# Performance work log

Measured on AMD Instinct MI355X. Metric: run time of the kernel, lower is better.

Reference implementation:

```python
import math
import jax, jax.numpy as jnp
import numpy as np

B, A, U, S, E, HYP, H = 16384, 32, 64, 2048, 32, 64, 4
ATTEND_REG_COEF = 1e-3


def setup_inputs() -> dict:
    key = jax.random.key(0)
    ks = jax.random.split(key, 12)
    sc = 0.05
    return {
        "agent_qs": jax.random.normal(ks[0], (B, A), jnp.float32),
        "states": jax.random.normal(ks[1], (B, S), jnp.float32),
        # per-head selector hypernet: Linear(S,HYP)+ReLU+Linear(HYP,E,no bias)
        "sel_w1": jax.random.normal(ks[2], (H, S, HYP), jnp.float32) * sc,
        "sel_b1": jax.random.normal(ks[3], (H, HYP), jnp.float32) * sc,
        "sel_w2": jax.random.normal(ks[4], (H, HYP, E), jnp.float32) * sc,
        # per-head key extractor: Linear(U,E,no bias)
        "key_w": jax.random.normal(ks[5], (H, U, E), jnp.float32) * sc,
        # V net: Linear(S,E)+ReLU+Linear(E,1)
        "v_w1": jax.random.normal(ks[6], (S, E), jnp.float32) * sc,
        "v_b1": jax.random.normal(ks[7], (E,), jnp.float32) * sc,
        "v_w2": jax.random.normal(ks[8], (E, 1), jnp.float32) * sc,
        "v_b2": jax.random.normal(ks[9], (1,), jnp.float32) * sc,
    }


def reference(agent_qs, states, sel_w1, sel_b1, sel_w2, key_w, v_w1, v_b1, v_w2, v_b2):
    # nonlinear=False, weighted_head=False, state_bias=True (defaults used here)
    unit_states = states[:, : A * U].reshape(-1, A, U)  # [B, A, U]

    # per-head selectors: [B, H, E]
    h1 = jax.nn.relu(jnp.einsum("bs,hsk->bhk", states, sel_w1) + sel_b1[None])
    selectors = jnp.einsum("bhk,hke->bhe", h1, sel_w2)

    # per-head, per-agent keys: [B, H, A, E]
    keys = jnp.einsum("bau,hue->bhae", unit_states, key_w)

    # attention logits [B, H, A] (matches selector @ stacked-keys in torch)
    logits = jnp.einsum("bhe,bhae->bha", selectors, keys)
    weights = jax.nn.softmax(logits / math.sqrt(E), axis=-1)  # [B, H, A]

    head_attend = jnp.sum(weights, axis=1)  # [B, A]

    v = jax.nn.relu(states @ v_w1 + v_b1) @ v_w2 + v_b2  # [B, 1]

    # coef * sum over heads of mean(logits_h ** 2)
    attend_mag_regs = ATTEND_REG_COEF * jnp.sum(jnp.mean(logits ** 2, axis=(0, 2)))

    # per-head entropy: -(p * log(p + 1e-8)).sum(agents).mean(batch) -> [H]
    head_entropies = -jnp.mean(
        jnp.sum(weights * jnp.log(weights + 1e-8), axis=-1), axis=0
    )

    return head_attend, v, attend_mag_regs, head_entropies
```

## Files before the change

### kernel.cpp

```cpp
#include <hip/hip_runtime.h>
#include <hip/hip_bf16.h>

#define B_N 16384
#define A_N 32
#define U_N 64
#define S_N 2048
#define E_N 32
#define HYP_N 64
#define H_N 4
#define NREAL 288
#define NPADG 320

#define WS_WT    0
#define WS_MB    1310720
#define WS_PMAG  (WS_MB + 32768)
#define WS_PENT  (WS_PMAG + 65536)

#define OUT_V   (B_N * A_N)
#define OUT_MAG (OUT_V + B_N)
#define OUT_ENT (OUT_MAG + 1)

typedef __attribute__((ext_vector_type(8))) short bf16x8_t;
typedef __attribute__((ext_vector_type(4))) float floatx4_t;

#define AS1(p) ((const __attribute__((address_space(1))) void*)(p))
#define AS3(p) ((__attribute__((address_space(3))) void*)(p))

__device__ __forceinline__ unsigned short f2b(float f) {
    union { float f; unsigned u; } v; v.f = f;
    unsigned r = v.u + 0x7FFFu + ((v.u >> 16) & 1u);
    return (unsigned short)(r >> 16);
}
__device__ __forceinline__ float b2f(unsigned x) {
    union { unsigned u; float f; } v; v.u = x << 16; return v.f;
}

__global__ __launch_bounds__(256) void pack_w_kernel(
        const float* __restrict__ sel_w1, const float* __restrict__ v_w1,
        const float* __restrict__ sel_w2, const float* __restrict__ key_w,
        unsigned short* __restrict__ Wt, unsigned short* __restrict__ Mb) {
    int idx = blockIdx.x * 256 + threadIdx.x;
    if (idx < NPADG * S_N) {
        int n = idx >> 11;
        int k = idx & 2047;
        float val = 0.0f;
        if (n < 256) {
            int h = n >> 6, kk = n & 63;
            val = sel_w1[((size_t)h * S_N + k) * HYP_N + kk];
        } else if (n < NREAL) {
            val = v_w1[(size_t)k * E_N + (n - 256)];
        }
        Wt[idx] = f2b(val);
    } else if (idx < NPADG * S_N + H_N * U_N * HYP_N) {
        int j = idx - NPADG * S_N;
        int h = j >> 12, u = (j >> 6) & 63, k = j & 63;
        const float* kw = key_w + ((size_t)h * U_N + u) * E_N;
        const float* w2 = sel_w2 + ((size_t)h * HYP_N + k) * E_N;
        float s = 0.0f;
#pragma unroll
        for (int e = 0; e < E_N; ++e) s = fmaf(kw[e], w2[e], s);
        Mb[j] = f2b(s);
    }
}

#define FM_BM 32
#define FM_BK 64
#define H1_STRIDE 312
#define TS_STRIDE 260

__global__ __launch_bounds__(256) void fused_kernel(
        const float* __restrict__ states, const unsigned short* __restrict__ Wt,
        const float* __restrict__ sel_b1, const float* __restrict__ v_b1,
        const unsigned short* __restrict__ Mb,
        const float* __restrict__ v_w2, const float* __restrict__ v_b2,
        float* __restrict__ out, float* __restrict__ pmag, float* __restrict__ pent) {
    __shared__ __align__(16) char pool[4096 + 40960 + H1_STRIDE * FM_BM * 2];
    unsigned short* Asm = (unsigned short*)pool;
    unsigned short* Bsm = (unsigned short*)(pool + 4096);
    float*          tsb = (float*)(pool + 4096);
    unsigned short* h1b = (unsigned short*)(pool + 4096 + 40960);

    const int t = threadIdx.x;
    const int lane = t & 63;
    const int w = t >> 6;
    const int m0 = blockIdx.x * FM_BM;
    const int nw = w * 80;

    const int ar = t >> 3, acl = t & 7;
    const float* ap = states + (size_t)(m0 + ar) * S_N + acl * 8;

    floatx4_t acc[2][5] = {};

    float4 a0 = *(const float4*)(ap);
    float4 a1 = *(const float4*)(ap + 4);
    {
        int ph = acl ^ (ar & 7);
        uint4 o;
        o.x = (unsigned)f2b(a0.x) | ((unsigned)f2b(a0.y) << 16);
        o.y = (unsigned)f2b(a0.z) | ((unsigned)f2b(a0.w) << 16);
        o.z = (unsigned)f2b(a1.x) | ((unsigned)f2b(a1.y) << 16);
        o.w = (unsigned)f2b(a1.z) | ((unsigned)f2b(a1.w) << 16);
        *(uint4*)(Asm + (size_t)(ar * 8 + ph) * 8) = o;
    }
#pragma unroll
    for (int i = 0; i < 10; ++i) {
        int p = i * 256 + t, n = p >> 3, sl = p & 7;
        int cl = sl ^ (n & 7);
        __builtin_amdgcn_global_load_lds(AS1(Wt + (size_t)n * S_N + cl * 8),
                                         AS3(Bsm + p * 8), 16, 0, 0);
    }
    __syncthreads();

    for (int it = 0; it < 32; ++it) {
        if (it < 31) {
            const float* g = ap + (it + 1) * FM_BK;
            a0 = *(const float4*)(g);
            a1 = *(const float4*)(g + 4);
        }
#pragma unroll
        for (int s = 0; s < 2; ++s) {
            const int c = s * 4 + (lane >> 4);
            bf16x8_t afr[2];
#pragma unroll
            for (int mt = 0; mt < 2; ++mt) {
                int r = mt * 16 + (lane & 15);
                int ph = c ^ (r & 7);
                afr[mt] = *(const bf16x8_t*)(Asm + r * 64 + ph * 8);
            }
#pragma unroll
            for (int nt = 0; nt < 5; ++nt) {
                int n = nw + nt * 16 + (lane & 15);
                int ph = c ^ (n & 7);
                bf16x8_t bfr = *(const bf16x8_t*)(Bsm + n * 64 + ph * 8);
                acc[0][nt] = __builtin_amdgcn_mfma_f32_16x16x32_bf16(
                    afr[0], bfr, acc[0][nt], 0, 0, 0);
                acc[1][nt] = __builtin_amdgcn_mfma_f32_16x16x32_bf16(
                    afr[1], bfr, acc[1][nt], 0, 0, 0);
            }
        }
        __syncthreads();
        if (it < 31) {
            int k0 = (it + 1) * FM_BK;
            {
                int ph = acl ^ (ar & 7);
                uint4 o;
                o.x = (unsigned)f2b(a0.x) | ((unsigned)f2b(a0.y) << 16);
                o.y = (unsigned)f2b(a0.z) | ((unsigned)f2b(a0.w) << 16);
                o.z = (unsigned)f2b(a1.x) | ((unsigned)f2b(a1.y) << 16);
                o.w = (unsigned)f2b(a1.z) | ((unsigned)f2b(a1.w) << 16);
                *(uint4*)(Asm + (size_t)(ar * 8 + ph) * 8) = o;
            }
#pragma unroll
            for (int i = 0; i < 10; ++i) {
                int p = i * 256 + t, n = p >> 3, sl = p & 7;
                int cl = sl ^ (n & 7);
                __builtin_amdgcn_global_load_lds(
                    AS1(Wt + (size_t)n * S_N + k0 + cl * 8),
                    AS3(Bsm + p * 8), 16, 0, 0);
            }
            __syncthreads();
        }
    }

#pragma unroll
    for (int nt = 0; nt < 5; ++nt) {
        int n = nw + nt * 16 + (lane & 15);
        if (n >= NREAL) continue;
        float bias = (n < 256) ? sel_b1[n] : v_b1[n - 256];
        int slot = (n < 256) ? ((n >> 6) * 72 + (n & 63))
                             : (((n - 256) >> 3) * 72 + 64 + ((n - 256) & 7));
#pragma unroll
        for (int mt = 0; mt < 2; ++mt) {
#pragma unroll
            for (int rg = 0; rg < 4; ++rg) {
                int r = mt * 16 + (lane >> 4) * 4 + rg;
                float v = acc[mt][nt][rg] + bias;
                h1b[r * H1_STRIDE + slot] = f2b(v > 0.0f ? v : 0.0f);
            }
        }
    }
    __syncthreads();

    {
        const int h = w;
        floatx4_t tacc[2][4] = {};
#pragma unroll
        for (int s = 0; s < 2; ++s) {
            int k0 = s * 32 + (lane >> 4) * 8;
            bf16x8_t bfr[4];
#pragma unroll
            for (int ut = 0; ut < 4; ++ut) {
                int u = ut * 16 + (lane & 15);
                bfr[ut] = *(const bf16x8_t*)(Mb + ((size_t)(h * U_N + u) * 64) + k0);
            }
#pragma unroll
            for (int mt = 0; mt < 2; ++mt) {
                int r = mt * 16 + (lane & 15);
                bf16x8_t afr = *(const bf16x8_t*)(h1b + r * H1_STRIDE + h * 72 + k0);
#pragma unroll
                for (int ut = 0; ut < 4; ++ut)
                    tacc[mt][ut] = __builtin_amdgcn_mfma_f32_16x16x32_bf16(
                        afr, bfr[ut], tacc[mt][ut], 0, 0, 0);
            }
        }
#pragma unroll
        for (int mt = 0; mt < 2; ++mt)
#pragma unroll
            for (int ut = 0; ut < 4; ++ut)
#pragma unroll
                for (int rg = 0; rg < 4; ++rg) {
                    int r = mt * 16 + (lane >> 4) * 4 + rg;
                    int u = ut * 16 + (lane & 15);
                    tsb[r * TS_STRIDE + h * U_N + u] = tacc[mt][ut][rg];
                }
    }
    __syncthreads();

    const int a = lane & 31, uh = lane >> 5;
    float4 cur[8], nxt[8];
    {
        const float* up = states + (size_t)(m0 + w * 8) * S_N + a * 64 + uh * 32;
#pragma unroll
        for (int i = 0; i < 8; ++i) cur[i] = ((const float4*)up)[i];
    }
    for (int rr = 0; rr < 8; ++rr) {
        int r = w * 8 + rr;
        int b = m0 + r;
        if (rr < 7) {
            const float* up = states + (size_t)(b + 1) * S_N + a * 64 + uh * 32;
#pragma unroll
            for (int i = 0; i < 8; ++i) nxt[i] = ((const float4*)up)[i];
        }
        float pl[4];
#pragma unroll
        for (int h = 0; h < 4; ++h) {
            const float* tp = &tsb[r * TS_STRIDE + h * U_N + uh * 32];
            float s = 0.0f;
#pragma unroll
            for (int i = 0; i < 8; ++i) {
                float4 t4 = *(const float4*)(tp + i * 4);
                s = fmaf(cur[i].x, t4.x, s);
                s = fmaf(cur[i].y, t4.y, s);
                s = fmaf(cur[i].z, t4.z, s);
                s = fmaf(cur[i].w, t4.w, s);
            }
            pl[h] = s + __shfl_xor(s, 32, 64);
        }
        float mg = pl[0]*pl[0] + pl[1]*pl[1] + pl[2]*pl[2] + pl[3]*pl[3];
#pragma unroll
        for (int o = 16; o > 0; o >>= 1) mg += __shfl_xor(mg, o, 32);
        float hatt = 0.0f;
        float entv[4];
#pragma unroll
        for (int h = 0; h < 4; ++h) {
            float x = pl[h] * 0.17677669529663687f;
            float m = x;
#pragma unroll
            for (int o = 16; o > 0; o >>= 1) m = fmaxf(m, __shfl_xor(m, o, 32));
            float p = expf(x - m);
            float den = p;
#pragma unroll
            for (int o = 16; o > 0; o >>= 1) den += __shfl_xor(den, o, 32);
            float wv = p / den;
            hatt += wv;
            float e = wv * logf(wv + 1e-8f);
#pragma unroll
            for (int o = 16; o > 0; o >>= 1) e += __shfl_xor(e, o, 32);
            entv[h] = e;
        }
        if (uh == 0) {
            out[(size_t)b * A_N + a] = hatt;
            float pv = b2f((unsigned)h1b[r * H1_STRIDE + (a >> 3) * 72 + 64 + (a & 7)])
                       * v_w2[a];
#pragma unroll
            for (int o = 16; o > 0; o >>= 1) pv += __shfl_xor(pv, o, 32);
            if (a == 0) {
                out[OUT_V + b] = pv + v_b2[0];
                pmag[b] = mg;
#pragma unroll
                for (int h = 0; h < 4; ++h) pent[(size_t)h * B_N + b] = entv[h];
            }
        }
#pragma unroll
        for (int i = 0; i < 8; ++i) cur[i] = nxt[i];
    }
}

__global__ __launch_bounds__(256) void finalize_kernel(
        const float* __restrict__ pmag, const float* __restrict__ pent,
        float* __restrict__ out) {
    int which = blockIdx.x;
    const float* src = (which == 0) ? pmag : (pent + (size_t)(which - 1) * B_N);
    float s = 0.0f;
    for (int i = threadIdx.x; i < B_N; i += 256) s += src[i];
#pragma unroll
    for (int o = 32; o > 0; o >>= 1) s += __shfl_xor(s, o, 64);
    __shared__ float red[4];
    if ((threadIdx.x & 63) == 0) red[threadIdx.x >> 6] = s;
    __syncthreads();
    if (threadIdx.x == 0) {
        float tot = red[0] + red[1] + red[2] + red[3];
        if (which == 0) out[OUT_MAG] = 1e-3f * tot / (float)(B_N * A_N);
        else out[OUT_ENT + which - 1] = -tot / (float)B_N;
    }
}

extern "C" void kernel_launch(void* const* d_in, const int* in_sizes, int n_in,
                              void* d_out, int out_size, void* d_ws, size_t ws_size,
                              hipStream_t stream) {
    const float* states = (const float*)d_in[1];
    const float* sel_w1 = (const float*)d_in[2];
    const float* sel_b1 = (const float*)d_in[3];
    const float* sel_w2 = (const float*)d_in[4];
    const float* key_w  = (const float*)d_in[5];
    const float* v_w1   = (const float*)d_in[6];
    const float* v_b1   = (const float*)d_in[7];
    const float* v_w2   = (const float*)d_in[8];
    const float* v_b2   = (const float*)d_in[9];
    float* out = (float*)d_out;
    char* wsb  = (char*)d_ws;

    unsigned short* Wt  = (unsigned short*)(wsb + WS_WT);
    unsigned short* Mb  = (unsigned short*)(wsb + WS_MB);
    float* pmag         = (float*)(wsb + WS_PMAG);
    float* pent         = (float*)(wsb + WS_PENT);

    pack_w_kernel<<<dim3((NPADG * S_N + H_N * U_N * HYP_N + 255) / 256),
                    dim3(256), 0, stream>>>(sel_w1, v_w1, sel_w2, key_w, Wt, Mb);
    fused_kernel<<<dim3(B_N / FM_BM), dim3(256), 0, stream>>>(
        states, Wt, sel_b1, v_b1, Mb, v_w2, v_b2, out, pmag, pent);
    finalize_kernel<<<dim3(5), dim3(256), 0, stream>>>(pmag, pent, out);
}
```

Baseline: 286.2 us.

## Double-buffer GEMM K-tiles with halved BK and one barrier per iteration

The main GEMM loop now uses a K tile of 32 instead of 64 and double-buffers both the A and B tiles in LDS, so the next tile's global-to-LDS loads are issued before the current tile's MFMAs. The two __syncthreads per iteration become a single custom barrier that waits with vmcnt(2), leaving the prefetched A register loads in flight. Only half of the threads load A, and the XOR swizzle is redone for 32-wide rows. The goal is to hide global load latency behind compute, at the cost of twice as many iterations with less MFMA work each and a hand-tuned waitcnt that depends on how the compiler orders memory operations.

New measurement: 311.7 us. 1.09x slower.

```diff
diff --git a/kernel.cpp b/kernel.cpp
--- a/kernel.cpp
+++ b/kernel.cpp
@@ -33,6 +33,13 @@
 }
 __device__ __forceinline__ float b2f(unsigned x) {
     union { unsigned u; float f; } v; v.u = x << 16; return v.f;
+}
+
+__device__ __forceinline__ void pipe_barrier(bool deep) {
+    if (deep) asm volatile("s_waitcnt vmcnt(2) lgkmcnt(0)" ::: "memory");
+    else      asm volatile("s_waitcnt vmcnt(0) lgkmcnt(0)" ::: "memory");
+    __builtin_amdgcn_s_barrier();
+    asm volatile("" ::: "memory");
 }
 
 __global__ __launch_bounds__(256) void pack_w_kernel(
@@ -64,7 +71,8 @@
 }
 
 #define FM_BM 32
-#define FM_BK 64
+#define FM_BK 32
+#define NIT   (S_N / FM_BK)
 #define H1_STRIDE 312
 #define TS_STRIDE 260
 
@@ -85,81 +93,85 @@
     const int w = t >> 6;
     const int m0 = blockIdx.x * FM_BM;
     const int nw = w * 80;
-
-    const int ar = t >> 3, acl = t & 7;
-    const float* ap = states + (size_t)(m0 + ar) * S_N + acl * 8;
+    const bool aduty = (t < 128);
+
+    const int ar = t >> 2, acl = t & 3;
+    const int asrc = acl ^ ((ar >> 1) & 3);
+    const float* ap = states + (size_t)(m0 + ar) * S_N + asrc * 8;
 
     floatx4_t acc[2][5] = {};
-
-    float4 a0 = *(const float4*)(ap);
-    float4 a1 = *(const float4*)(ap + 4);
-    {
-        int ph = acl ^ (ar & 7);
+    float4 av0, av1;
+
+    if (aduty) { av0 = *(const float4*)ap; av1 = *(const float4*)(ap + 4); }
+#pragma unroll
+    for (int i = 0; i < 5; ++i) {
+        int q = i * 256 + t, n = q >> 2, cl = q & 3;
+        int so = cl ^ ((n >> 1) & 3);
+        __builtin_amdgcn_global_load_lds(AS1(Wt + (size_t)n * S_N + so * 8),
+                                         AS3(Bsm + q * 8), 16, 0, 0);
+    }
+    if (aduty) {
         uint4 o;
-        o.x = (unsigned)f2b(a0.x) | ((unsigned)f2b(a0.y) << 16);
-        o.y = (unsigned)f2b(a0.z) | ((unsigned)f2b(a0.w) << 16);
-        o.z = (unsigned)f2b(a1.x) | ((unsigned)f2b(a1.y) << 16);
-        o.w = (unsigned)f2b(a1.z) | ((unsigned)f2b(a1.w) << 16);
-        *(uint4*)(Asm + (size_t)(ar * 8 + ph) * 8) = o;
-    }
-#pragma unroll
-    for (int i = 0; i < 10; ++i) {
-        int p = i * 256 + t, n = p >> 3, sl = p & 7;
-        int cl = sl ^ (n & 7);
-        __builtin_amdgcn_global_load_lds(AS1(Wt + (size_t)n * S_N + cl * 8),
-                                         AS3(Bsm + p * 8), 16, 0, 0);
-    }
-    __syncthreads();
-
-    for (int it = 0; it < 32; ++it) {
-        if (it < 31) {
-            const float* g = ap + (it + 1) * FM_BK;
-            a0 = *(const float4*)(g);
-            a1 = *(const float4*)(g + 4);
-        }
-#pragma unroll
-        for (int s = 0; s < 2; ++s) {
-            const int c = s * 4 + (lane >> 4);
+        o.x = (unsigned)f2b(av0.x) | ((unsigned)f2b(av0.y) << 16);
+        o.y = (unsigned)f2b(av0.z) | ((unsigned)f2b(av0.w) << 16);
+        o.z = (unsigned)f2b(av1.x) | ((unsigned)f2b(av1.y) << 16);
+        o.w = (unsigned)f2b(av1.z) | ((unsigned)f2b(av1.w) << 16);
+        *(uint4*)(Asm + (ar * 4 + acl) * 8) = o;
+        av0 = *(const float4*)(ap + FM_BK);
+        av1 = *(const float4*)(ap + FM_BK + 4);
+    }
+    pipe_barrier(aduty);
+
+#pragma unroll 2
+    for (int it = 0; it < NIT; ++it) {
+        const int p = it & 1;
+        unsigned short* As = Asm + p * 1024;
+        unsigned short* Bs = Bsm + p * 10240;
+        if (it < NIT - 1) {
+            unsigned short* Bn = Bsm + (p ^ 1) * 10240;
+            const int k0 = (it + 1) * FM_BK;
+#pragma unroll
+            for (int i = 0; i < 5; ++i) {
+                int q = i * 256 + t, n = q >> 2, cl = q & 3;
+                int so = cl ^ ((n >> 1) & 3);
+                __builtin_amdgcn_global_load_lds(
+                    AS1(Wt + (size_t)n * S_N + k0 + so * 8),
+                    AS3(Bn + q * 8), 16, 0, 0);
+            }
+            if (aduty) {
+                unsigned short* An = Asm + (p ^ 1) * 1024;
+                uint4 o;
+                o.x = (unsigned)f2b(av0.x) | ((unsigned)f2b(av0.y) << 16);
+                o.y = (unsigned)f2b(av0.z) | ((unsigned)f2b(av0.w) << 16);
+                o.z = (unsigned)f2b(av1.x) | ((unsigned)f2b(av1.y) << 16);
+                o.w = (unsigned)f2b(av1.z) | ((unsigned)f2b(av1.w) << 16);
+                *(uint4*)(An + (ar * 4 + acl) * 8) = o;
+                if (it < NIT - 2) {
+                    const float* g = ap + (it + 2) * FM_BK;
+                    av0 = *(const float4*)g;
+                    av1 = *(const float4*)(g + 4);
+                }
+            }
+        }
+        {
+            const int c = lane >> 4;
             bf16x8_t afr[2];
 #pragma unroll
             for (int mt = 0; mt < 2; ++mt) {
                 int r = mt * 16 + (lane & 15);
-                int ph = c ^ (r & 7);
-                afr[mt] = *(const bf16x8_t*)(Asm + r * 64 + ph * 8);
+                afr[mt] = *(const bf16x8_t*)(As + r * 32 + ((c ^ ((r >> 1) & 3)) * 8));
             }
 #pragma unroll
             for (int nt = 0; nt < 5; ++nt) {
                 int n = nw + nt * 16 + (lane & 15);
-                int ph = c ^ (n & 7);
-                bf16x8_t bfr = *(const bf16x8_t*)(Bsm + n * 64 + ph * 8);
+                bf16x8_t bfr = *(const bf16x8_t*)(Bs + n * 32 + ((c ^ ((n >> 1) & 3)) * 8));
                 acc[0][nt] = __builtin_amdgcn_mfma_f32_16x16x32_bf16(
                     afr[0], bfr, acc[0][nt], 0, 0, 0);
                 acc[1][nt] = __builtin_amdgcn_mfma_f32_16x16x32_bf16(
                     afr[1], bfr, acc[1][nt], 0, 0, 0);
             }
         }
-        __syncthreads();
-        if (it < 31) {
-            int k0 = (it + 1) * FM_BK;
-            {
-                int ph = acl ^ (ar & 7);
-                uint4 o;
-                o.x = (unsigned)f2b(a0.x) | ((unsigned)f2b(a0.y) << 16);
-                o.y = (unsigned)f2b(a0.z) | ((unsigned)f2b(a0.w) << 16);
-                o.z = (unsigned)f2b(a1.x) | ((unsigned)f2b(a1.y) << 16);
-                o.w = (unsigned)f2b(a1.z) | ((unsigned)f2b(a1.w) << 16);
-                *(uint4*)(Asm + (size_t)(ar * 8 + ph) * 8) = o;
-            }
-#pragma unroll
-            for (int i = 0; i < 10; ++i) {
-                int p = i * 256 + t, n = p >> 3, sl = p & 7;
-                int cl = sl ^ (n & 7);
-                __builtin_amdgcn_global_load_lds(
-                    AS1(Wt + (size_t)n * S_N + k0 + cl * 8),
-                    AS3(Bsm + p * 8), 16, 0, 0);
-            }
-            __syncthreads();
-        }
+        if (it < NIT - 1) pipe_barrier(aduty && it < NIT - 2);
     }
 
 #pragma unroll
```

## Stream B weights directly into registers and double-buffer larger A chunks in LDS

Applied to the files above, without the earlier changes.

The GEMM main loop is restructured. B (packed weight) fragments are now loaded straight from global memory into registers, double-buffered per k-step, instead of being staged through LDS with global_load_lds. The states tile is processed in 256-wide K chunks with a double-buffered LDS A buffer, which cuts barriers from two per 64-K step to one per 256-K chunk. Launch bounds request 2 blocks per CU and LDS is shrunk to allow it. The cost is that B reads hit global/L2 directly with less coalescing, and register pressure rises from the prefetched A and B fragments.

Measured after the change: 332.6 us. 1.16x slower.

```diff
diff --git a/kernel.cpp b/kernel.cpp
--- a/kernel.cpp
+++ b/kernel.cpp
@@ -22,9 +22,6 @@
 
 typedef __attribute__((ext_vector_type(8))) short bf16x8_t;
 typedef __attribute__((ext_vector_type(4))) float floatx4_t;
-
-#define AS1(p) ((const __attribute__((address_space(1))) void*)(p))
-#define AS3(p) ((__attribute__((address_space(3))) void*)(p))
 
 __device__ __forceinline__ unsigned short f2b(float f) {
     union { float f; unsigned u; } v; v.f = f;
@@ -64,21 +61,22 @@
 }
 
 #define FM_BM 32
-#define FM_BK 64
+#define CHK 256
+#define NCHK (S_N / CHK)
+#define KSC (CHK / 32)
 #define H1_STRIDE 312
 #define TS_STRIDE 260
 
-__global__ __launch_bounds__(256) void fused_kernel(
+__global__ __launch_bounds__(256, 2) void fused_kernel(
         const float* __restrict__ states, const unsigned short* __restrict__ Wt,
         const float* __restrict__ sel_b1, const float* __restrict__ v_b1,
         const unsigned short* __restrict__ Mb,
         const float* __restrict__ v_w2, const float* __restrict__ v_b2,
         float* __restrict__ out, float* __restrict__ pmag, float* __restrict__ pent) {
-    __shared__ __align__(16) char pool[4096 + 40960 + H1_STRIDE * FM_BM * 2];
-    unsigned short* Asm = (unsigned short*)pool;
-    unsigned short* Bsm = (unsigned short*)(pool + 4096);
-    float*          tsb = (float*)(pool + 4096);
-    unsigned short* h1b = (unsigned short*)(pool + 4096 + 40960);
+    __shared__ __align__(16) char pool[53248];
+    unsigned short* Abuf = (unsigned short*)pool;
+    unsigned short* h1b  = (unsigned short*)pool;
+    float*          tsb  = (float*)(pool + 19968);
 
     const int t = threadIdx.x;
     const int lane = t & 63;
@@ -86,80 +84,75 @@
     const int m0 = blockIdx.x * FM_BM;
     const int nw = w * 80;
 
-    const int ar = t >> 3, acl = t & 7;
-    const float* ap = states + (size_t)(m0 + ar) * S_N + acl * 8;
+    const int ar = t >> 3, aq = t & 7;
+    const float* abase = states + (size_t)(m0 + ar) * S_N + aq * 32;
 
     floatx4_t acc[2][5] = {};
-
-    float4 a0 = *(const float4*)(ap);
-    float4 a1 = *(const float4*)(ap + 4);
-    {
-        int ph = acl ^ (ar & 7);
-        uint4 o;
-        o.x = (unsigned)f2b(a0.x) | ((unsigned)f2b(a0.y) << 16);
-        o.y = (unsigned)f2b(a0.z) | ((unsigned)f2b(a0.w) << 16);
-        o.z = (unsigned)f2b(a1.x) | ((unsigned)f2b(a1.y) << 16);
-        o.w = (unsigned)f2b(a1.z) | ((unsigned)f2b(a1.w) << 16);
-        *(uint4*)(Asm + (size_t)(ar * 8 + ph) * 8) = o;
-    }
-#pragma unroll
-    for (int i = 0; i < 10; ++i) {
-        int p = i * 256 + t, n = p >> 3, sl = p & 7;
-        int cl = sl ^ (n & 7);
-        __builtin_amdgcn_global_load_lds(AS1(Wt + (size_t)n * S_N + cl * 8),
-                                         AS3(Bsm + p * 8), 16, 0, 0);
-    }
+    float4 avn[8];
+    bf16x8_t bq[2][5];
+    const int bn15 = lane & 15, bko = (lane >> 4) * 8;
+
+    auto loadA = [&](int ch) {
+        const float* g = abase + ch * CHK;
+#pragma unroll
+        for (int i = 0; i < 8; ++i) avn[i] = ((const float4*)g)[i];
+    };
+    auto writeA = [&](unsigned short* dst) {
+#pragma unroll
+        for (int j = 0; j < 4; ++j) {
+            int o = aq * 4 + j;
+            int ph = (o & 24) | ((o & 7) ^ (ar & 7));
+            uint4 u;
+            u.x = (unsigned)f2b(avn[2*j].x)   | ((unsigned)f2b(avn[2*j].y)   << 16);
+            u.y = (unsigned)f2b(avn[2*j].z)   | ((unsigned)f2b(avn[2*j].w)   << 16);
+            u.z = (unsigned)f2b(avn[2*j+1].x) | ((unsigned)f2b(avn[2*j+1].y) << 16);
+            u.w = (unsigned)f2b(avn[2*j+1].z) | ((unsigned)f2b(avn[2*j+1].w) << 16);
+            *(uint4*)(dst + ar * 256 + ph * 8) = u;
+        }
+    };
+    auto loadB = [&](bf16x8_t* q, int ksg) {
+#pragma unroll
+        for (int nt = 0; nt < 5; ++nt) {
+            int n = nw + nt * 16 + bn15;
+            q[nt] = *(const bf16x8_t*)(Wt + (size_t)n * S_N + ksg * 32 + bko);
+        }
+    };
+
+    loadA(0);
+    writeA(Abuf);
+    loadA(1);
+    loadB(bq[0], 0);
+    loadB(bq[1], 1);
     __syncthreads();
 
-    for (int it = 0; it < 32; ++it) {
-        if (it < 31) {
-            const float* g = ap + (it + 1) * FM_BK;
-            a0 = *(const float4*)(g);
-            a1 = *(const float4*)(g + 4);
-        }
-#pragma unroll
-        for (int s = 0; s < 2; ++s) {
-            const int c = s * 4 + (lane >> 4);
-            bf16x8_t afr[2];
+#pragma unroll 1
+    for (int chunk = 0; chunk < NCHK; ++chunk) {
+        unsigned short* As = Abuf + (chunk & 1) * 8192;
+        if (chunk < NCHK - 1) {
+            writeA(Abuf + ((chunk & 1) ^ 1) * 8192);
+            if (chunk < NCHK - 2) loadA(chunk + 2);
+        }
+#pragma unroll
+        for (int ks = 0; ks < KSC; ++ks) {
+            bf16x8_t af[2];
 #pragma unroll
             for (int mt = 0; mt < 2; ++mt) {
                 int r = mt * 16 + (lane & 15);
-                int ph = c ^ (r & 7);
-                afr[mt] = *(const bf16x8_t*)(Asm + r * 64 + ph * 8);
+                int o = ks * 4 + (lane >> 4);
+                int ph = (o & 24) | ((o & 7) ^ (r & 7));
+                af[mt] = *(const bf16x8_t*)(As + r * 256 + ph * 8);
             }
 #pragma unroll
             for (int nt = 0; nt < 5; ++nt) {
-                int n = nw + nt * 16 + (lane & 15);
-                int ph = c ^ (n & 7);
-                bf16x8_t bfr = *(const bf16x8_t*)(Bsm + n * 64 + ph * 8);
                 acc[0][nt] = __builtin_amdgcn_mfma_f32_16x16x32_bf16(
-                    afr[0], bfr, acc[0][nt], 0, 0, 0);
+                    af[0], bq[ks & 1][nt], acc[0][nt], 0, 0, 0);
                 acc[1][nt] = __builtin_amdgcn_mfma_f32_16x16x32_bf16(
-                    afr[1], bfr, acc[1][nt], 0, 0, 0);
-            }
+                    af[1], bq[ks & 1][nt], acc[1][nt], 0, 0, 0);
+            }
+            if (ks < KSC - 2 || chunk < NCHK - 1)
+                loadB(bq[ks & 1], chunk * KSC + ks + 2);
         }
         __syncthreads();
-        if (it < 31) {
-            int k0 = (it + 1) * FM_BK;
-            {
-                int ph = acl ^ (ar & 7);
-                uint4 o;
-                o.x = (unsigned)f2b(a0.x) | ((unsigned)f2b(a0.y) << 16);
-                o.y = (unsigned)f2b(a0.z) | ((unsigned)f2b(a0.w) << 16);
-                o.z = (unsigned)f2b(a1.x) | ((unsigned)f2b(a1.y) << 16);
-                o.w = (unsigned)f2b(a1.z) | ((unsigned)f2b(a1.w) << 16);
-                *(uint4*)(Asm + (size_t)(ar * 8 + ph) * 8) = o;
-            }
-#pragma unroll
-            for (int i = 0; i < 10; ++i) {
-                int p = i * 256 + t, n = p >> 3, sl = p & 7;
-                int cl = sl ^ (n & 7);
-                __builtin_amdgcn_global_load_lds(
-                    AS1(Wt + (size_t)n * S_N + k0 + cl * 8),
-                    AS3(Bsm + p * 8), 16, 0, 0);
-            }
-            __syncthreads();
-        }
     }
 
 #pragma unroll
```

## Use 512-thread blocks splitting M tile across wave pairs, deepen A prefetch

Applied to the files above, without the earlier changes.

Doubles the block to 8 waves, each wave now owning 16 rows by 80 columns instead of 32 by 80, which halves accumulators per wave and spreads the attention epilogue rows over more waves. The states A-tile prefetch is moved so the next-next tile loads during the current store phase. The aim is to raise wave occupancy and latency hiding on the bandwidth-bound GEMM, but each wave now issues half the MFMAs per B-fragment load, raising LDS read traffic per flop. Downstream stages are remapped so the epilogue and per-row loop work with 8 waves.

Result: faster. 279.3 us (-2.4%).

```diff
diff --git a/kernel.cpp b/kernel.cpp
--- a/kernel.cpp
+++ b/kernel.cpp
@@ -65,10 +65,11 @@
 
 #define FM_BM 32
 #define FM_BK 64
+#define NIT   (S_N / FM_BK)
 #define H1_STRIDE 312
 #define TS_STRIDE 260
 
-__global__ __launch_bounds__(256) void fused_kernel(
+__global__ __launch_bounds__(512, 4) void fused_kernel(
         const float* __restrict__ states, const unsigned short* __restrict__ Wt,
         const float* __restrict__ sel_b1, const float* __restrict__ v_b1,
         const unsigned short* __restrict__ Mb,
@@ -84,16 +85,18 @@
     const int lane = t & 63;
     const int w = t >> 6;
     const int m0 = blockIdx.x * FM_BM;
-    const int nw = w * 80;
+    const int miw = (w & 1) * 16;
+    const int nw = (w >> 1) * 80;
 
     const int ar = t >> 3, acl = t & 7;
     const float* ap = states + (size_t)(m0 + ar) * S_N + acl * 8;
 
-    floatx4_t acc[2][5] = {};
-
-    float4 a0 = *(const float4*)(ap);
-    float4 a1 = *(const float4*)(ap + 4);
-    {
+    floatx4_t acc[5] = {};
+    float4 a0, a1;
+
+    if (t < 256) {
+        a0 = *(const float4*)(ap);
+        a1 = *(const float4*)(ap + 4);
         int ph = acl ^ (ar & 7);
         uint4 o;
         o.x = (unsigned)f2b(a0.x) | ((unsigned)f2b(a0.y) << 16);
@@ -103,45 +106,38 @@
         *(uint4*)(Asm + (size_t)(ar * 8 + ph) * 8) = o;
     }
 #pragma unroll
-    for (int i = 0; i < 10; ++i) {
-        int p = i * 256 + t, n = p >> 3, sl = p & 7;
+    for (int i = 0; i < 5; ++i) {
+        int p = i * 512 + t, n = p >> 3, sl = p & 7;
         int cl = sl ^ (n & 7);
         __builtin_amdgcn_global_load_lds(AS1(Wt + (size_t)n * S_N + cl * 8),
                                          AS3(Bsm + p * 8), 16, 0, 0);
     }
+    if (t < 256) {
+        a0 = *(const float4*)(ap + FM_BK);
+        a1 = *(const float4*)(ap + FM_BK + 4);
+    }
     __syncthreads();
 
-    for (int it = 0; it < 32; ++it) {
-        if (it < 31) {
-            const float* g = ap + (it + 1) * FM_BK;
-            a0 = *(const float4*)(g);
-            a1 = *(const float4*)(g + 4);
-        }
+    for (int it = 0; it < NIT; ++it) {
 #pragma unroll
         for (int s = 0; s < 2; ++s) {
             const int c = s * 4 + (lane >> 4);
-            bf16x8_t afr[2];
-#pragma unroll
-            for (int mt = 0; mt < 2; ++mt) {
-                int r = mt * 16 + (lane & 15);
-                int ph = c ^ (r & 7);
-                afr[mt] = *(const bf16x8_t*)(Asm + r * 64 + ph * 8);
-            }
+            int r = miw + (lane & 15);
+            int pha = c ^ (r & 7);
+            bf16x8_t afr = *(const bf16x8_t*)(Asm + r * 64 + pha * 8);
 #pragma unroll
             for (int nt = 0; nt < 5; ++nt) {
                 int n = nw + nt * 16 + (lane & 15);
                 int ph = c ^ (n & 7);
                 bf16x8_t bfr = *(const bf16x8_t*)(Bsm + n * 64 + ph * 8);
-                acc[0][nt] = __builtin_amdgcn_mfma_f32_16x16x32_bf16(
-                    afr[0], bfr, acc[0][nt], 0, 0, 0);
-                acc[1][nt] = __builtin_amdgcn_mfma_f32_16x16x32_bf16(
-                    afr[1], bfr, acc[1][nt], 0, 0, 0);
+                acc[nt] = __builtin_amdgcn_mfma_f32_16x16x32_bf16(
+                    afr, bfr, acc[nt], 0, 0, 0);
             }
         }
         __syncthreads();
-        if (it < 31) {
+        if (it < NIT - 1) {
             int k0 = (it + 1) * FM_BK;
-            {
+            if (t < 256) {
                 int ph = acl ^ (ar & 7);
                 uint4 o;
                 o.x = (unsigned)f2b(a0.x) | ((unsigned)f2b(a0.y) << 16);
@@ -151,12 +147,17 @@
                 *(uint4*)(Asm + (size_t)(ar * 8 + ph) * 8) = o;
             }
 #pragma unroll
-            for (int i = 0; i < 10; ++i) {
-                int p = i * 256 + t, n = p >> 3, sl = p & 7;
+            for (int i = 0; i < 5; ++i) {
+                int p = i * 512 + t, n = p >> 3, sl = p & 7;
                 int cl = sl ^ (n & 7);
                 __builtin_amdgcn_global_load_lds(
                     AS1(Wt + (size_t)n * S_N + k0 + cl * 8),
                     AS3(Bsm + p * 8), 16, 0, 0);
+            }
+            if (it < NIT - 2 && t < 256) {
+                const float* g = ap + (it + 2) * FM_BK;
+                a0 = *(const float4*)(g);
+                a1 = *(const float4*)(g + 4);
             }
             __syncthreads();
         }
@@ -170,63 +171,53 @@
         int slot = (n < 256) ? ((n >> 6) * 72 + (n & 63))
                              : (((n - 256) >> 3) * 72 + 64 + ((n - 256) & 7));
 #pragma unroll
-        for (int mt = 0; mt < 2; ++mt) {
-#pragma unroll
-            for (int rg = 0; rg < 4; ++rg) {
-                int r = mt * 16 + (lane >> 4) * 4 + rg;
-                float v = acc[mt][nt][rg] + bias;
-                h1b[r * H1_STRIDE + slot] = f2b(v > 0.0f ? v : 0.0f);
-            }
+        for (int rg = 0; rg < 4; ++rg) {
+            int r = miw + (lane >> 4) * 4 + rg;
+            float v = acc[nt][rg] + bias;
+            h1b[r * H1_STRIDE + slot] = f2b(v > 0.0f ? v : 0.0f);
         }
     }
     __syncthreads();
 
     {
-        const int h = w;
-        floatx4_t tacc[2][4] = {};
+        const int h = w >> 1;
+        const int rb = (w & 1) * 16;
+        floatx4_t tacc[4] = {};
 #pragma unroll
         for (int s = 0; s < 2; ++s) {
             int k0 = s * 32 + (lane >> 4) * 8;
-            bf16x8_t bfr[4];
+            bf16x8_t afr = *(const bf16x8_t*)(h1b + (rb + (lane & 15)) * H1_STRIDE
+                                              + h * 72 + k0);
 #pragma unroll
             for (int ut = 0; ut < 4; ++ut) {
                 int u = ut * 16 + (lane & 15);
-                bfr[ut] = *(const bf16x8_t*)(Mb + ((size_t)(h * U_N + u) * 64) + k0);
-            }
-#pragma unroll
-            for (int mt = 0; mt < 2; ++mt) {
-                int r = mt * 16 + (lane & 15);
-                bf16x8_t afr = *(const bf16x8_t*)(h1b + r * H1_STRIDE + h * 72 + k0);
-#pragma unroll
-                for (int ut = 0; ut < 4; ++ut)
-                    tacc[mt][ut] = __builtin_amdgcn_mfma_f32_16x16x32_bf16(
-                        afr, bfr[ut], tacc[mt][ut], 0, 0, 0);
-            }
-        }
-#pragma unroll
-        for (int mt = 0; mt < 2; ++mt)
-#pragma unroll
-            for (int ut = 0; ut < 4; ++ut)
-#pragma unroll
-                for (int rg = 0; rg < 4; ++rg) {
-                    int r = mt * 16 + (lane >> 4) * 4 + rg;
-                    int u = ut * 16 + (lane & 15);
-                    tsb[r * TS_STRIDE + h * U_N + u] = tacc[mt][ut][rg];
-                }
+                bf16x8_t bfr = *(const bf16x8_t*)(Mb + ((size_t)(h * U_N + u) * 64) + k0);
+                tacc[ut] = __builtin_amdgcn_mfma_f32_16x16x32_bf16(
+                    afr, bfr, tacc[ut], 0, 0, 0);
+            }
+        }
+#pragma unroll
+        for (int ut = 0; ut < 4; ++ut)
+#pragma unroll
+            for (int rg = 0; rg < 4; ++rg) {
+                int r = rb + (lane >> 4) * 4 + rg;
+                int u = ut * 16 + (lane & 15);
+                tsb[r * TS_STRIDE + h * U_N + u] = tacc[ut][rg];
+            }
     }
     __syncthreads();
 
     const int a = lane & 31, uh = lane >> 5;
     float4 cur[8], nxt[8];
     {
-        const float* up = states + (size_t)(m0 + w * 8) * S_N + a * 64 + uh * 32;
+        const float* up = states + (size_t)(m0 + w * 4) * S_N + a * 64 + uh * 32;
 #pragma unroll
         for (int i = 0; i < 8; ++i) cur[i] = ((const float4*)up)[i];
     }
-    for (int rr = 0; rr < 8; ++rr) {
-        int r = w * 8 + rr;
+    for (int rr = 0; rr < 4; ++rr) {
+        int r = w * 4 + rr;
         int b = m0 + r;
-        if (rr < 7) {
+        if (rr < 3) {
             const float* up = states + (size_t)(b + 1) * S_N + a * 64 + uh * 32;
 #pragma unroll
             for (int i = 0; i < 8; ++i) nxt[i] = ((const float4*)up)[i];
@@ -327,7 +318,7 @@
 
     pack_w_kernel<<<dim3((NPADG * S_N + H_N * U_N * HYP_N + 255) / 256),
                     dim3(256), 0, stream>>>(sel_w1, v_w1, sel_w2, key_w, Wt, Mb);
-    fused_kernel<<<dim3(B_N / FM_BM), dim3(256), 0, stream>>>(
+    fused_kernel<<<dim3(B_N / FM_BM), dim3(512), 0, stream>>>(
         states, Wt, sel_b1, v_b1, Mb, v_w2, v_b2, out, pmag, pent);
     finalize_kernel<<<dim3(5), dim3(256), 0, stream>>>(pmag, pent, out);
 }
```
